# Performance work log

Measured on AMD Instinct MI355X. Metric: run time of the kernel, lower is better.

## Reference

```python
import jax, jax.numpy as jnp
import numpy as np

B, S, D = 2, 2048, 2048
H, KVH = 16, 4
HD = D // H  # 128


def _rope_angles(seq, head_dim):
    theta = 1.0 / (10000.0 ** (jnp.arange(0, head_dim, 2, dtype=jnp.float32) / head_dim))
    ang = jnp.arange(seq, dtype=jnp.float32)[:, None] * theta[None, :]  # [S, HD/2]
    return jnp.cos(ang), jnp.sin(ang)


def _apply_rotary(t, cos, sin):
    # t: [B, S, h, HD]; pairs are (even, odd) along last dim (view_as_complex semantics)
    tr = t[..., 0::2]
    ti = t[..., 1::2]
    c = cos[None, :, None, :]
    s = sin[None, :, None, :]
    out_r = tr * c - ti * s
    out_i = tr * s + ti * c
    return jnp.stack([out_r, out_i], axis=-1).reshape(t.shape)


def setup_inputs() -> dict:
    key = jax.random.key(0)
    ks = jax.random.split(key, 8)
    sd = 1.0 / np.sqrt(D)
    return {
        'x': jax.random.normal(ks[0], (B, S, D), dtype=jnp.float32),
        'wq': jax.random.normal(ks[1], (D, D), dtype=jnp.float32) * sd,
        'bq': jax.random.normal(ks[2], (D,), dtype=jnp.float32) * 0.01,
        'wk': jax.random.normal(ks[3], (D, KVH * HD), dtype=jnp.float32) * sd,
        'bk': jax.random.normal(ks[4], (KVH * HD,), dtype=jnp.float32) * 0.01,
        'wv': jax.random.normal(ks[5], (D, KVH * HD), dtype=jnp.float32) * sd,
        'bv': jax.random.normal(ks[6], (KVH * HD,), dtype=jnp.float32) * 0.01,
        'wo': jax.random.normal(ks[7], (D, D), dtype=jnp.float32) * sd,
    }


def reference(x, wq, bq, wk, bk, wv, bv, wo):
    b, s, d = x.shape
    q = (x @ wq + bq).reshape(b, s, H, HD)
    k = (x @ wk + bk).reshape(b, s, KVH, HD)
    v = (x @ wv + bv).reshape(b, s, KVH, HD)

    cos, sin = _rope_angles(s, HD)
    q = _apply_rotary(q, cos, sin)
    k = _apply_rotary(k, cos, sin)

    repeat = H // KVH
    k = jnp.repeat(k, repeat, axis=2)  # [B, S, H, HD]
    v = jnp.repeat(v, repeat, axis=2)

    scale = 1.0 / np.sqrt(HD)
    att_score = jnp.einsum('bqhd,bkhd->bqhk', q, k) * scale  # [B, S, H, S]
    att_weight = jax.nn.softmax(att_score, axis=-1)
    out = jnp.einsum('bqhk,bkhd->bqhd', att_weight, v)
    out = out.reshape(b, s, H * HD)
    return out @ wo
```

## Files before the change

kernel.cpp:

```cpp
#include <hip/hip_runtime.h>
#include <hip/hip_bf16.h>
#include <cstdint>

typedef __attribute__((ext_vector_type(4))) float f32x4;
typedef __attribute__((ext_vector_type(16))) float f32x16;
typedef __attribute__((ext_vector_type(8))) short bf16x8;
typedef __attribute__((ext_vector_type(4))) unsigned int u32x4;
typedef unsigned short u16;
typedef unsigned int u32;

__device__ __forceinline__ u16 f2b(float x) {
  __hip_bfloat16 h = __float2bfloat16(x);
  return *reinterpret_cast<u16*>(&h);
}

__device__ __forceinline__ u32 pk(float a, float b) {
  return ((u32)f2b(b) << 16) | (u32)f2b(a);
}

__device__ __forceinline__ void gload16(const void* g, void* l) {
  __builtin_amdgcn_global_load_lds((const __attribute__((address_space(1))) u32*)g,
                                   (__attribute__((address_space(3))) u32*)l, 16, 0, 0);
}

__device__ __forceinline__ float xmax32(float x) {
  return fmaxf(x, __shfl_xor(x, 32, 64));
}
__device__ __forceinline__ float xsum32(float x) {
  return x + __shfl_xor(x, 32, 64);
}


__global__ void cvt_f32_bf16(const float* __restrict__ in, u16* __restrict__ out, int n4) {
  int idx = (blockIdx.x * 256 + threadIdx.x);
  if (idx < n4) {
    const float4 v = *(const float4*)(in + (size_t)idx * 4);
    u16* o = out + (size_t)idx * 4;
    o[0] = f2b(v.x); o[1] = f2b(v.y); o[2] = f2b(v.z); o[3] = f2b(v.w);
  }
}

__global__ void w_transpose_cvt(const float* __restrict__ w0, const float* __restrict__ w1,
                                const float* __restrict__ w2, int b0, int b1,
                                int N0, int N1, int N2,
                                u16* __restrict__ out, int K) {
  __shared__ float tile[32][33];
  int k0 = blockIdx.x * 32, n0 = blockIdx.y * 32;
  const float* src; int srcN; int c0;
  if (n0 < b0)      { src = w0; srcN = N0; c0 = n0; }
  else if (n0 < b1) { src = w1; srcN = N1; c0 = n0 - b0; }
  else              { src = w2; srcN = N2; c0 = n0 - b1; }
  int tx = threadIdx.x & 31, ty = threadIdx.x >> 5;
#pragma unroll
  for (int j = 0; j < 32; j += 8)
    tile[ty + j][tx] = src[(size_t)(k0 + ty + j) * srcN + c0 + tx];
  __syncthreads();
#pragma unroll
  for (int j = 0; j < 32; j += 8)
    out[(size_t)(n0 + ty + j) * K + k0 + tx] = f2b(tile[tx][ty + j]);
}

__global__ void pack_bias(const float* __restrict__ bq, const float* __restrict__ bk,
                          const float* __restrict__ bv, float* __restrict__ out) {
  int i = blockIdx.x * 256 + threadIdx.x;
  if (i < 3072) out[i] = (i < 2048) ? bq[i] : ((i < 2560) ? bk[i - 2048] : bv[i - 2560]);
}

__global__ void v_transpose_cvt(const float* __restrict__ qkv, u16* __restrict__ vt) {
  __shared__ float tile[32][33];
  int s0 = blockIdx.x * 32;
  int d0 = blockIdx.y * 32;
  int z = blockIdx.z;
  int b = z >> 2, kvh = z & 3;
  int tx = threadIdx.x & 31, ty = threadIdx.x >> 5;
#pragma unroll
  for (int j = 0; j < 32; j += 8)
    tile[ty + j][tx] = qkv[((size_t)(b * 2048 + s0 + ty + j)) * 3072 + 2560 + kvh * 128 + d0 + tx];
  __syncthreads();
#pragma unroll
  for (int j = 0; j < 32; j += 8)
    vt[((size_t)z * 128 + d0 + ty + j) * 2048 + s0 + tx] = f2b(tile[tx][ty + j]);
}

__global__ void rope_cvt(const float* __restrict__ qkv, u16* __restrict__ out,
                         int lognh, int col0, float scale) {
  int idx = blockIdx.x * 256 + threadIdx.x;
  int i = idx & 63;
  int nh = 1 << lognh;
  int h = (idx >> 6) & (nh - 1);
  int bs = idx >> (6 + lognh);
  int s = bs & 2047;
  int b = bs >> 11;
  const float* src = qkv + (size_t)bs * 3072 + col0 + h * 128 + 2 * i;
  float tr = src[0], ti = src[1];
  float theta = expf(-(float)i * 0.14391156831212787f);
  float ang = (float)s * theta;
  float sv, cv;
  sincosf(ang, &sv, &cv);
  float orr = (tr * cv - ti * sv) * scale;
  float oii = (tr * sv + ti * cv) * scale;
  u16* dst = out + (((size_t)(b * nh + h) * 2048 + s) * 128 + 2 * i);
  dst[0] = f2b(orr);
  dst[1] = f2b(oii);
}

__global__ __launch_bounds__(256) void gemm_bt_bf16(
    const u16* __restrict__ A, const u16* __restrict__ Bt,
    const float* __restrict__ bias, float* __restrict__ C,
    int M, int N, int K) {
  __shared__ u16 As[128 * 32];
  __shared__ u16 Bs[128 * 32];
  const int tid = threadIdx.x;
  const int lane = tid & 63;
  const int w = tid >> 6;
  const int wr = w >> 1, wc = w & 1;
  const int m0 = blockIdx.y * 128;
  const int n0 = blockIdx.x * 128;

  f32x4 acc[4][4] = {};

  for (int k0 = 0; k0 < K; k0 += 32) {
#pragma unroll
    for (int it = 0; it < 2; ++it) {
      int c = tid + it * 256;
      int row = c >> 2;
      int off = (c & 3) * 8;
      gload16(A + (size_t)(m0 + row) * K + k0 + off, (u16*)As + w * 512 + it * 2048);
      gload16(Bt + (size_t)(n0 + row) * K + k0 + off, (u16*)Bs + w * 512 + it * 2048);
    }
    __syncthreads();
    const int col8 = (lane >> 4) * 8;
    bf16x8 a[4], bfr[4];
#pragma unroll
    for (int m = 0; m < 4; ++m)
      a[m] = *(const bf16x8*)&As[(wr * 64 + m * 16 + (lane & 15)) * 32 + col8];
#pragma unroll
    for (int n = 0; n < 4; ++n)
      bfr[n] = *(const bf16x8*)&Bs[(wc * 64 + n * 16 + (lane & 15)) * 32 + col8];
#pragma unroll
    for (int m = 0; m < 4; ++m)
#pragma unroll
      for (int n = 0; n < 4; ++n)
        acc[m][n] = __builtin_amdgcn_mfma_f32_16x16x32_bf16(a[m], bfr[n], acc[m][n], 0, 0, 0);
    __syncthreads();
  }

#pragma unroll
  for (int m = 0; m < 4; ++m) {
    int row = m0 + wr * 64 + m * 16 + ((lane >> 4) << 2);
#pragma unroll
    for (int n = 0; n < 4; ++n) {
      int col = n0 + wc * 64 + n * 16 + (lane & 15);
      float bvv = bias ? bias[col] : 0.f;
      float* cp = C + (size_t)row * N + col;
#pragma unroll
      for (int r = 0; r < 4; ++r) cp[(size_t)r * N] = acc[m][n][r] + bvv;
    }
  }
}

__global__ __launch_bounds__(128, 3) void flash_attn(
    const u16* __restrict__ Qr, const u16* __restrict__ Kr,
    const u16* __restrict__ Vt, u16* __restrict__ Att) {
  __shared__ u16 Ks[2][32 * 128];
  __shared__ u16 Vs[2][128 * 32];
  const int tid = threadIdx.x, lane = tid & 63, w = tid >> 6;
  const int lo = lane & 31, hi = lane >> 5;
  const int q0 = blockIdx.x * 64 + w * 32;
  const int h = blockIdx.y, b = blockIdx.z;
  const int kvh = h >> 2;

  const char* Khead = (const char*)(Kr + (size_t)(b * 4 + kvh) * 2048 * 128);
  const char* Vhead = (const char*)(Vt + (size_t)(b * 4 + kvh) * 128 * 2048);

  bf16x8 qf[8];
  {
    const u16* qp = Qr + ((size_t)(b * 16 + h) * 2048 + q0 + lo) * 128 + hi * 8;
#pragma unroll
    for (int ds = 0; ds < 8; ++ds) qf[ds] = *(const bf16x8*)(qp + ds * 16);
  }

#define STAGE(bufi, t)                                                        \
  {                                                                           \
    _Pragma("unroll")                                                         \
    for (int it = 0; it < 4; ++it) {                                          \
      int c = it * 128 + tid;                                                 \
      int krow = c >> 4;                                                      \
      int koff = krow * 256 + ((c & 15) << 4 ^ ((krow & 7) << 4));            \
      gload16(Khead + (size_t)(t) * 8192 + koff,                              \
              (u16*)Ks[bufi] + it * 1024 + w * 512);                          \
      int vrow = c >> 2;                                                      \
      int voff = vrow * 4096 + ((c & 3) << 4 ^ (((vrow >> 1) & 3) << 4));     \
      gload16(Vhead + (size_t)(t) * 64 + voff,                                \
              (u16*)Vs[bufi] + it * 1024 + w * 512);                          \
    }                                                                         \
  }

  f32x16 o0 = {}, o1 = {}, o2 = {}, o3 = {};
  float m_run = -3.0e38f, l_run = 0.f;
  const int swz = (lo & 7) << 4;
  const int vswz = ((lo >> 1) & 3) << 4;
  const int hi16 = hi * 16;

  STAGE(0, 0);
  __syncthreads();

  int buf = 0;
  for (int t = 0; t < 64; ++t) {
    int tn = (t < 63) ? t + 1 : 63;
    STAGE(buf ^ 1, tn);

    const char* Kb = (const char*)Ks[buf];
    const char* Vb = (const char*)Vs[buf];

    f32x16 sc = {};
    __builtin_amdgcn_s_setprio(1);
#pragma unroll
    for (int ds = 0; ds < 8; ++ds) {
      bf16x8 kf = *(const bf16x8*)(Kb + lo * 256 + ((ds * 32 + hi16) ^ swz));
      sc = __builtin_amdgcn_mfma_f32_32x32x16_bf16(kf, qf[ds], sc, 0, 0, 0);
    }
    __builtin_amdgcn_s_setprio(0);

    float m01 = fmaxf(fmaxf(sc[0], sc[1]), fmaxf(sc[2], sc[3]));
    float m23 = fmaxf(fmaxf(sc[4], sc[5]), fmaxf(sc[6], sc[7]));
    float m45 = fmaxf(fmaxf(sc[8], sc[9]), fmaxf(sc[10], sc[11]));
    float m67 = fmaxf(fmaxf(sc[12], sc[13]), fmaxf(sc[14], sc[15]));
    float pmax = xmax32(fmaxf(fmaxf(m01, m23), fmaxf(m45, m67)));

    if (!__all(pmax - m_run <= 8.0f)) {
      float mnew = fmaxf(m_run, pmax);
      float rs = __expf(m_run - mnew);
      m_run = mnew;
      l_run *= rs;
#pragma unroll
      for (int r = 0; r < 16; ++r) {
        float rsr = __shfl(rs, (r & 3) + 8 * (r >> 2) + 4 * hi, 64);
        o0[r] *= rsr; o1[r] *= rsr; o2[r] *= rsr; o3[r] *= rsr;
      }
    }

    float lsum = 0.f;
#pragma unroll
    for (int r = 0; r < 16; ++r) { float p = __expf(sc[r] - m_run); sc[r] = p; lsum += p; }
    l_run += xsum32(lsum);

    bf16x8 pa0, pa1;
    {
      u32 a0 = pk(sc[0], sc[1]),   a1 = pk(sc[2], sc[3]);
      u32 b0 = pk(sc[4], sc[5]),   b1 = pk(sc[6], sc[7]);
      u32 t0 = hi ? a0 : b0, t1 = hi ? a1 : b1;
      u32 r0 = __shfl_xor(t0, 32, 64), r1 = __shfl_xor(t1, 32, 64);
      u32x4 w0;
      w0[0] = hi ? r0 : a0; w0[1] = hi ? r1 : a1;
      w0[2] = hi ? b0 : r0; w0[3] = hi ? b1 : r1;
      pa0 = __builtin_bit_cast(bf16x8, w0);
      u32 c0 = pk(sc[8], sc[9]),   c1 = pk(sc[10], sc[11]);
      u32 d0 = pk(sc[12], sc[13]), d1 = pk(sc[14], sc[15]);
      u32 t2 = hi ? c0 : d0, t3 = hi ? c1 : d1;
      u32 r2 = __shfl_xor(t2, 32, 64), r3 = __shfl_xor(t3, 32, 64);
      u32x4 w1;
      w1[0] = hi ? r2 : c0; w1[1] = hi ? r3 : c1;
      w1[2] = hi ? d0 : r2; w1[3] = hi ? d1 : r3;
      pa1 = __builtin_bit_cast(bf16x8, w1);
    }

    __builtin_amdgcn_s_setprio(1);
#define PVN(on, n)                                                                                     \
    {                                                                                                  \
      const char* vrb = Vb + ((n) * 32 + lo) * 64;                                                     \
      on = __builtin_amdgcn_mfma_f32_32x32x16_bf16(pa0, *(const bf16x8*)(vrb + ((0  + hi16) ^ vswz)), on, 0, 0, 0); \
      on = __builtin_amdgcn_mfma_f32_32x32x16_bf16(pa1, *(const bf16x8*)(vrb + ((32 + hi16) ^ vswz)), on, 0, 0, 0); \
    }
    PVN(o0, 0)
    PVN(o1, 1)
    PVN(o2, 2)
    PVN(o3, 3)
    __builtin_amdgcn_s_setprio(0);

    __syncthreads();
    buf ^= 1;
  }

  float inv = 1.0f / l_run;
  size_t rowbase = (size_t)(b * 2048 + q0);
#pragma unroll
  for (int r = 0; r < 16; ++r) {
    int rr = (r & 3) + 8 * (r >> 2) + 4 * hi;
    float invr = __shfl(inv, rr, 64);
    u16* op = Att + (rowbase + rr) * 2048 + h * 128 + lo;
    op[0]  = f2b(o0[r] * invr);
    op[32] = f2b(o1[r] * invr);
    op[64] = f2b(o2[r] * invr);
    op[96] = f2b(o3[r] * invr);
  }
}


extern "C" void kernel_launch(void* const* d_in, const int* in_sizes, int n_in,
                              void* d_out, int out_size, void* d_ws, size_t ws_size,
                              hipStream_t stream) {
  const float* x  = (const float*)d_in[0];
  const float* wq = (const float*)d_in[1];
  const float* bq = (const float*)d_in[2];
  const float* wk = (const float*)d_in[3];
  const float* bk = (const float*)d_in[4];
  const float* wv = (const float*)d_in[5];
  const float* bv = (const float*)d_in[6];
  const float* wo = (const float*)d_in[7];
  float* out = (float*)d_out;
  char* ws = (char*)d_ws;

  u16*   x_bf   = (u16*)  (ws + 0);
  u16*   att    = (u16*)  (ws + 0);
  u16*   wqkv_t = (u16*)  (ws + 16777216);
  u16*   wo_t   = (u16*)  (ws + 29360128);
  float* biasq  = (float*)(ws + 37748736);
  float* qkv    = (float*)(ws + 37761024);
  u16*   q_r    = (u16*)  (ws + 88092672);
  u16*   k_r    = (u16*)  (ws + 104869888);
  u16*   v_t    = (u16*)  (ws + 109064192);

  cvt_f32_bf16<<<8192, 256, 0, stream>>>(x, x_bf, 2097152);
  w_transpose_cvt<<<dim3(64, 96), 256, 0, stream>>>(wq, wk, wv, 2048, 2560,
                                                    2048, 512, 512, wqkv_t, 2048);
  w_transpose_cvt<<<dim3(64, 64), 256, 0, stream>>>(wo, wo, wo, 2048, 2560,
                                                    2048, 2048, 2048, wo_t, 2048);
  pack_bias<<<12, 256, 0, stream>>>(bq, bk, bv, biasq);

  gemm_bt_bf16<<<dim3(24, 32), 256, 0, stream>>>(x_bf, wqkv_t, biasq, qkv, 4096, 3072, 2048);

  rope_cvt<<<16384, 256, 0, stream>>>(qkv, q_r, 4, 0, 0.08838834764831845f);
  rope_cvt<<<4096, 256, 0, stream>>>(qkv, k_r, 2, 2048, 1.0f);
  v_transpose_cvt<<<dim3(64, 4, 8), 256, 0, stream>>>(qkv, v_t);

  flash_attn<<<dim3(32, 16, 2), 128, 0, stream>>>(q_r, k_r, v_t, att);

  gemm_bt_bf16<<<dim3(16, 32), 256, 0, stream>>>(att, wo_t, nullptr, out, 4096, 2048, 2048);
}
```

Before: 294.6 us.

## Swizzle block order for XCD locality, fold log2e into Q scale, use exp2

The GEMM and flash-attention grids become 1D with a block-index swizzle. Consecutive blocks that run on the same XCD (blockIdx mod 8) then share operand tiles, and in attention they share the same KV head, which should raise L2 reuse. The Q pre-scale now includes log2(e), so softmax can use exp2f, and the rescale threshold is widened to match. Bf16 packing uses the paired conversion intrinsic. The accumulators are restructured into an array with the V loads hoisted. Together these are several independent tweaks, and the swizzle relies on the grid sizes dividing evenly by 8.

New measurement: 305.3 us. +3.6%, slower.

```diff
diff --git a/kernel.cpp b/kernel.cpp
--- a/kernel.cpp
+++ b/kernel.cpp
@@ -15,7 +15,8 @@
 }
 
 __device__ __forceinline__ u32 pk(float a, float b) {
-  return ((u32)f2b(b) << 16) | (u32)f2b(a);
+  __hip_bfloat162 h2 = __float22bfloat162_rn(float2{a, b});
+  return *reinterpret_cast<u32*>(&h2);
 }
 
 __device__ __forceinline__ void gload16(const void* g, void* l) {
@@ -107,15 +108,17 @@
 __global__ __launch_bounds__(256) void gemm_bt_bf16(
     const u16* __restrict__ A, const u16* __restrict__ Bt,
     const float* __restrict__ bias, float* __restrict__ C,
-    int M, int N, int K) {
+    int M, int N, int K, int gx) {
   __shared__ u16 As[128 * 32];
   __shared__ u16 Bs[128 * 32];
   const int tid = threadIdx.x;
   const int lane = tid & 63;
   const int w = tid >> 6;
   const int wr = w >> 1, wc = w & 1;
-  const int m0 = blockIdx.y * 128;
-  const int n0 = blockIdx.x * 128;
+  const int nb = gridDim.x;
+  const int swz = (blockIdx.x & 7) * (nb >> 3) + (blockIdx.x >> 3);
+  const int m0 = (swz / gx) * 128;
+  const int n0 = (swz % gx) * 128;
 
   f32x4 acc[4][4] = {};
 
@@ -166,9 +169,12 @@
   __shared__ u16 Vs[2][128 * 32];
   const int tid = threadIdx.x, lane = tid & 63, w = tid >> 6;
   const int lo = lane & 31, hi = lane >> 5;
-  const int q0 = blockIdx.x * 64 + w * 32;
-  const int h = blockIdx.y, b = blockIdx.z;
-  const int kvh = h >> 2;
+  const int bid = blockIdx.x;
+  const int g = bid & 7;
+  const int local = bid >> 3;
+  const int b = g >> 2, kvh = g & 3;
+  const int h = kvh * 4 + (local & 3);
+  const int q0 = (local >> 2) * 64 + w * 32;
 
   const char* Khead = (const char*)(Kr + (size_t)(b * 4 + kvh) * 2048 * 128);
   const char* Vhead = (const char*)(Vt + (size_t)(b * 4 + kvh) * 128 * 2048);
@@ -196,7 +202,7 @@
     }                                                                         \
   }
 
-  f32x16 o0 = {}, o1 = {}, o2 = {}, o3 = {};
+  f32x16 o0[4] = {};
   float m_run = -3.0e38f, l_run = 0.f;
   const int swz = (lo & 7) << 4;
   const int vswz = ((lo >> 1) & 3) << 4;
@@ -222,28 +228,29 @@
     }
     __builtin_amdgcn_s_setprio(0);
 
-    float m01 = fmaxf(fmaxf(sc[0], sc[1]), fmaxf(sc[2], sc[3]));
-    float m23 = fmaxf(fmaxf(sc[4], sc[5]), fmaxf(sc[6], sc[7]));
-    float m45 = fmaxf(fmaxf(sc[8], sc[9]), fmaxf(sc[10], sc[11]));
-    float m67 = fmaxf(fmaxf(sc[12], sc[13]), fmaxf(sc[14], sc[15]));
-    float pmax = xmax32(fmaxf(fmaxf(m01, m23), fmaxf(m45, m67)));
-
-    if (!__all(pmax - m_run <= 8.0f)) {
-      float mnew = fmaxf(m_run, pmax);
-      float rs = __expf(m_run - mnew);
-      m_run = mnew;
-      l_run *= rs;
-#pragma unroll
-      for (int r = 0; r < 16; ++r) {
-        float rsr = __shfl(rs, (r & 3) + 8 * (r >> 2) + 4 * hi, 64);
-        o0[r] *= rsr; o1[r] *= rsr; o2[r] *= rsr; o3[r] *= rsr;
+    {
+      float t0 = fmaxf(fmaxf(sc[0], sc[1]), sc[2]);
+      float t1 = fmaxf(fmaxf(sc[3], sc[4]), sc[5]);
+      float t2 = fmaxf(fmaxf(sc[6], sc[7]), sc[8]);
+      float t3 = fmaxf(fmaxf(sc[9], sc[10]), sc[11]);
+      float t4 = fmaxf(fmaxf(sc[12], sc[13]), sc[14]);
+      float pmax = xmax32(fmaxf(fmaxf(fmaxf(t0, t1), t2), fmaxf(fmaxf(t3, t4), sc[15])));
+      if (!__all(pmax - m_run <= 11.0f)) {
+        float mnew = fmaxf(m_run, pmax);
+        float rs = exp2f(m_run - mnew);
+        m_run = mnew;
+        l_run *= rs;
+#pragma unroll
+        for (int r = 0; r < 16; ++r) {
+          float rsr = __shfl(rs, (r & 3) + 8 * (r >> 2) + 4 * hi, 64);
+          o0[0][r] *= rsr; o0[1][r] *= rsr; o0[2][r] *= rsr; o0[3][r] *= rsr;
+        }
       }
-    }
-
-    float lsum = 0.f;
-#pragma unroll
-    for (int r = 0; r < 16; ++r) { float p = __expf(sc[r] - m_run); sc[r] = p; lsum += p; }
-    l_run += xsum32(lsum);
+      float lsum = 0.f;
+#pragma unroll
+      for (int r = 0; r < 16; ++r) { float p = exp2f(sc[r] - m_run); sc[r] = p; lsum += p; }
+      l_run += xsum32(lsum);
+    }
 
     bf16x8 pa0, pa1;
     {
@@ -266,16 +273,14 @@
     }
 
     __builtin_amdgcn_s_setprio(1);
-#define PVN(on, n)                                                                                     \
-    {                                                                                                  \
-      const char* vrb = Vb + ((n) * 32 + lo) * 64;                                                     \
-      on = __builtin_amdgcn_mfma_f32_32x32x16_bf16(pa0, *(const bf16x8*)(vrb + ((0  + hi16) ^ vswz)), on, 0, 0, 0); \
-      on = __builtin_amdgcn_mfma_f32_32x32x16_bf16(pa1, *(const bf16x8*)(vrb + ((32 + hi16) ^ vswz)), on, 0, 0, 0); \
-    }
-    PVN(o0, 0)
-    PVN(o1, 1)
-    PVN(o2, 2)
-    PVN(o3, 3)
+#pragma unroll
+    for (int n = 0; n < 4; ++n) {
+      const char* vrb = Vb + (n * 32 + lo) * 64;
+      bf16x8 vb0 = *(const bf16x8*)(vrb + ((0  + hi16) ^ vswz));
+      bf16x8 vb1 = *(const bf16x8*)(vrb + ((32 + hi16) ^ vswz));
+      o0[n] = __builtin_amdgcn_mfma_f32_32x32x16_bf16(pa0, vb0, o0[n], 0, 0, 0);
+      o0[n] = __builtin_amdgcn_mfma_f32_32x32x16_bf16(pa1, vb1, o0[n], 0, 0, 0);
+    }
     __builtin_amdgcn_s_setprio(0);
 
     __syncthreads();
@@ -289,10 +294,10 @@
     int rr = (r & 3) + 8 * (r >> 2) + 4 * hi;
     float invr = __shfl(inv, rr, 64);
     u16* op = Att + (rowbase + rr) * 2048 + h * 128 + lo;
-    op[0]  = f2b(o0[r] * invr);
-    op[32] = f2b(o1[r] * invr);
-    op[64] = f2b(o2[r] * invr);
-    op[96] = f2b(o3[r] * invr);
+    op[0]  = f2b(o0[0][r] * invr);
+    op[32] = f2b(o0[1][r] * invr);
+    op[64] = f2b(o0[2][r] * invr);
+    op[96] = f2b(o0[3][r] * invr);
   }
 }
 
@@ -328,13 +333,13 @@
                                                     2048, 2048, 2048, wo_t, 2048);
   pack_bias<<<12, 256, 0, stream>>>(bq, bk, bv, biasq);
 
-  gemm_bt_bf16<<<dim3(24, 32), 256, 0, stream>>>(x_bf, wqkv_t, biasq, qkv, 4096, 3072, 2048);
-
-  rope_cvt<<<16384, 256, 0, stream>>>(qkv, q_r, 4, 0, 0.08838834764831845f);
+  gemm_bt_bf16<<<768, 256, 0, stream>>>(x_bf, wqkv_t, biasq, qkv, 4096, 3072, 2048, 24);
+
+  rope_cvt<<<16384, 256, 0, stream>>>(qkv, q_r, 4, 0, 0.12751743871465216f);
   rope_cvt<<<4096, 256, 0, stream>>>(qkv, k_r, 2, 2048, 1.0f);
   v_transpose_cvt<<<dim3(64, 4, 8), 256, 0, stream>>>(qkv, v_t);
 
-  flash_attn<<<dim3(32, 16, 2), 128, 0, stream>>>(q_r, k_r, v_t, att);
-
-  gemm_bt_bf16<<<dim3(16, 32), 256, 0, stream>>>(att, wo_t, nullptr, out, 4096, 2048, 2048);
-}
+  flash_attn<<<1024, 128, 0, stream>>>(q_r, k_r, v_t, att);
+
+  gemm_bt_bf16<<<512, 256, 0, stream>>>(att, wo_t, nullptr, out, 4096, 2048, 2048, 16);
+}
```
